# Kernel optimization log

Hardware: AMD Instinct MI355X
Metric: run time of the kernel (lower is better)

Reference implementation:

```python
import jax, jax.numpy as jnp
import numpy as np

B, L, D, K = 32, 128, 400, 40
RTOL, ATOL = 1e-4, 1e-6


def setup_inputs() -> dict:
    key = jax.random.key(0)
    ks = jax.random.split(key, 9)
    s = 0.3                      # input scale keeps exp(energy) in fp32 range
    u = 1.0 / np.sqrt(D)         # param scale
    input_h = jax.random.normal(ks[0], (B, L, D), jnp.float32) * s
    input_c = jax.random.normal(ks[1], (B, L, D), jnp.float32) * s
    W_d = jax.random.normal(ks[2], (K, D), jnp.float32) * u
    W_e = jax.random.normal(ks[3], (K, D), jnp.float32) * u
    U = jax.random.normal(ks[4], (K, D, D), jnp.float32) * u
    b = jax.random.normal(ks[5], (K,), jnp.float32) * 0.1
    heads = jax.random.randint(ks[6], (B, L), 0, L)
    pos = jnp.arange(L)[None, :]
    heads = jnp.where(heads == pos, (heads + 1) % L, heads)  # no self-loops (diag is -inf)
    arc_tags = jax.random.randint(ks[7], (B, L), 0, K)
    lengths = jax.random.randint(ks[8], (B,), L // 2, L + 1)
    mask = (jnp.arange(L)[None, :] < lengths[:, None]).astype(jnp.float32)
    return {"input_h": input_h, "input_c": input_c, "W_d": W_d, "W_e": W_e,
            "U": U, "b": b, "mask": mask, "heads": heads,
            "arc_tags": arc_tags, "lengths": lengths}


def reference(input_h, input_c, W_d, W_e, U, b, mask, heads, arc_tags, lengths):
    Bsz, Ln, _ = input_h.shape
    # --- BiAAttention: energy[b,k,head,child] ---
    bil = jnp.einsum('bhd,kde,bce->bkhc', input_h, U, input_c)
    sd = jnp.einsum('kd,bhd->bkh', W_d, input_h)[:, :, :, None]   # head bias
    se = jnp.einsum('kd,bcd->bkc', W_e, input_c)[:, :, None, :]   # child bias
    energy = bil + sd + se + b[None, :, None, None]
    energy = energy * mask[:, None, :, None] * mask[:, None, None, :]
    eye = jnp.eye(Ln, dtype=energy.dtype)
    energy = energy + jnp.where(eye > 0, -jnp.inf, 0.0)           # no self-arcs
    # --- Matrix-Tree partition function ---
    A = jnp.exp(energy) * mask[:, None, :, None] * mask[:, None, None, :]
    A = A.sum(axis=1)                                             # [B,L,L] over labels
    Dg = A.sum(axis=1) * (1.0 + RTOL) + ATOL                      # column (in-degree) sums
    Lap = eye * Dg[:, None, :] - A                                # Laplacian
    Sub = Lap[:, 1:, 1:]                                          # drop root row/col
    valid = jnp.arange(Ln - 1)[None, :] < (lengths - 1)[:, None]
    vm = valid[:, :, None] & valid[:, None, :]
    Sub = jnp.where(vm, Sub, jnp.eye(Ln - 1, dtype=Sub.dtype))    # identity-pad = logdet of [1:len,1:len]
    z = jnp.linalg.slogdet(Sub)[1]                                # [B]
    # --- gold-tree energy ---
    bi = jnp.arange(Bsz)[:, None]
    pos = jnp.arange(Ln)[None, :]
    te = energy[bi, arc_tags, heads, pos]                         # [B,L]
    tgt = te[:, 1:].sum(axis=1)
    return z - tgt
```

## Files before the change

### kernel.cpp

```cpp
#include <hip/hip_runtime.h>
#include <hip/hip_bf16.h>

#define BB 32
#define LL 128
#define DD 400
#define KK 40
#define EE 416
#define SDN 50
#define SEN 52

typedef __attribute__((ext_vector_type(8)))  short  bfrag;
typedef __attribute__((ext_vector_type(16))) float  ffrag;

static __device__ __forceinline__ short f2bf(float f) {
    union { float f; unsigned u; } v; v.f = f;
    unsigned r = (v.u + 0x7FFF + ((v.u >> 16) & 1)) >> 16;
    return (short)r;
}

__global__ __launch_bounds__(256) void p_hc(
    const float* __restrict__ H, const float* __restrict__ C,
    short* __restrict__ Hs, short* __restrict__ Cs)
{
    int id = blockIdx.x * 256 + threadIdx.x;
    if (id < BB*SDN*LL) {
        int b = id / (SDN*LL); int r = id % (SDN*LL);
        int sd = r / LL; int h = r % LL;
        const float* src = H + ((size_t)(b*LL + h))*DD + sd*8;
        bfrag v;
#pragma unroll
        for (int j = 0; j < 8; ++j) v[j] = f2bf(src[j]);
        *(bfrag*)(Hs + (size_t)id*8) = v;
    } else {
        id -= BB*SDN*LL;
        int b = id / (SEN*LL); int r = id % (SEN*LL);
        int se = r / LL; int c = r % LL;
        bfrag v;
#pragma unroll
        for (int j = 0; j < 8; ++j) {
            int e = se*8 + j;
            v[j] = (e < DD) ? f2bf(C[((size_t)(b*LL + c))*DD + e]) : (short)0;
        }
        *(bfrag*)(Cs + (size_t)id*8) = v;
    }
}

__global__ __launch_bounds__(256) void p_u(
    const float* __restrict__ U, short* __restrict__ Us)
{
    int id = blockIdx.x * 256 + threadIdx.x;
    int k = id / (SDN*EE); int r = id % (SDN*EE);
    int sd = r / EE; int e = r % EE;
    bfrag v;
#pragma unroll
    for (int j = 0; j < 8; ++j)
        v[j] = (e < DD) ? f2bf(U[((size_t)k*DD + sd*8 + j)*DD + e]) : (short)0;
    *(bfrag*)(Us + (size_t)id*8) = v;
}

__global__ __launch_bounds__(256) void k_sdse(
    const float* __restrict__ H, const float* __restrict__ C,
    const float* __restrict__ Wd, const float* __restrict__ We,
    float* __restrict__ SD, float* __restrict__ SE)
{
    const int k = blockIdx.x % KK;
    const int b = blockIdx.x / KK;
    const int t = threadIdx.x;
    __shared__ float wd[DD], we[DD];
    for (int f = t; f < DD; f += 256) { wd[f] = Wd[k*DD + f]; we[f] = We[k*DD + f]; }
    __syncthreads();
    const int row = t & 127;
    const float* src = (t < 128) ? (H + (size_t)(b*LL + row)*DD)
                                 : (C + (size_t)(b*LL + row)*DD);
    const float* w = (t < 128) ? wd : we;
    float s = 0.f;
    for (int d = 0; d < DD; d += 4) {
        float4 v = *(const float4*)(src + d);
        s = fmaf(v.x, w[d+0], s); s = fmaf(v.y, w[d+1], s);
        s = fmaf(v.z, w[d+2], s); s = fmaf(v.w, w[d+3], s);
    }
    if (t < 128) SD[(b*KK + k)*LL + row] = s;
    else         SE[(b*KK + k)*LL + row] = s;
}

__global__ __launch_bounds__(256, 2) void k_mfma(
    const short* __restrict__ Hs, const short* __restrict__ Cs,
    const short* __restrict__ Us,
    const float* __restrict__ SD, const float* __restrict__ SE,
    const float* __restrict__ bvec, const float* __restrict__ mask,
    const int* __restrict__ heads, const int* __restrict__ tags,
    float* __restrict__ A8, float* __restrict__ tgt)
{
    const int k = blockIdx.x;
    const int b = blockIdx.y;
    const int t = threadIdx.x;
    const int w  = t >> 6;
    const int l  = t & 63;
    const int l31 = l & 31;
    const int kh  = l >> 5;
    const int wm  = w >> 1;
    const int wn  = w & 1;

    __shared__ short Tbuf[16*LL*8];

    ffrag Sacc[2][2];
#pragma unroll
    for (int a = 0; a < 2; ++a)
#pragma unroll
        for (int c2 = 0; c2 < 2; ++c2)
#pragma unroll
            for (int r = 0; r < 16; ++r) Sacc[a][c2][r] = 0.f;

    const size_t usK = (size_t)k * SDN * EE;
    const size_t hsB = (size_t)b * SDN * LL;
    const size_t csB = (size_t)b * SEN * LL;

    for (int chunk = 0; chunk < 4; ++chunk) {
        const int e0  = chunk * 128;
        const int NEc = (chunk < 3) ? 128 : 32;
        const int nmt = (NEc == 128) ? 2 : ((wm == 0) ? 1 : 0);

        ffrag Tacc[2][2];
#pragma unroll
        for (int a = 0; a < 2; ++a)
#pragma unroll
            for (int c2 = 0; c2 < 2; ++c2)
#pragma unroll
                for (int r = 0; r < 16; ++r) Tacc[a][c2][r] = 0.f;

        if (nmt > 0) {
            for (int ds = 0; ds < 25; ++ds) {
                const int sdl = 2*ds + kh;
                bfrag afr[2], bfr[2];
#pragma unroll
                for (int mt = 0; mt < 2; ++mt) {
                    if (mt < nmt) {
                        int eg = e0 + 64*wm + 32*mt + l31;
                        afr[mt] = *(const bfrag*)(Us + (usK + (size_t)sdl*EE + eg)*8);
                    }
                }
#pragma unroll
                for (int nt = 0; nt < 2; ++nt) {
                    int h = 64*wn + 32*nt + l31;
                    bfr[nt] = *(const bfrag*)(Hs + (hsB + (size_t)sdl*LL + h)*8);
                }
#pragma unroll
                for (int mt = 0; mt < 2; ++mt) {
                    if (mt < nmt) {
#pragma unroll
                        for (int nt = 0; nt < 2; ++nt)
                            Tacc[mt][nt] = __builtin_amdgcn_mfma_f32_32x32x16_bf16(
                                afr[mt], bfr[nt], Tacc[mt][nt], 0, 0, 0);
                    }
                }
            }
#pragma unroll
            for (int mt = 0; mt < 2; ++mt) {
                if (mt < nmt) {
#pragma unroll
                    for (int nt = 0; nt < 2; ++nt) {
                        int h = 64*wn + 32*nt + l31;
#pragma unroll
                        for (int r = 0; r < 16; r += 2) {
                            int e_loc = 64*wm + 32*mt + (r&3) + 8*(r>>2) + 4*kh;
                            int s_e = e_loc >> 3, e7 = e_loc & 7;
                            unsigned lo = (unsigned short)f2bf(Tacc[mt][nt][r]);
                            unsigned hi = (unsigned short)f2bf(Tacc[mt][nt][r+1]);
                            *(unsigned*)(&Tbuf[((size_t)s_e*LL + h)*8 + e7]) =
                                lo | (hi << 16);
                        }
                    }
                }
            }
        }
        __syncthreads();

        const int esteps = NEc >> 4;
        for (int es = 0; es < esteps; ++es) {
            const int sel = 2*es + kh;
            bfrag afr[2], bfr[2];
#pragma unroll
            for (int at = 0; at < 2; ++at) {
                int h = 64*wm + 32*at + l31;
                afr[at] = *(const bfrag*)(&Tbuf[((size_t)sel*LL + h)*8]);
            }
#pragma unroll
            for (int bt = 0; bt < 2; ++bt) {
                int c = 64*wn + 32*bt + l31;
                int seg = (e0 >> 3) + sel;
                bfr[bt] = *(const bfrag*)(Cs + (csB + (size_t)seg*LL + c)*8);
            }
#pragma unroll
            for (int at = 0; at < 2; ++at)
#pragma unroll
                for (int bt = 0; bt < 2; ++bt)
                    Sacc[at][bt] = __builtin_amdgcn_mfma_f32_32x32x16_bf16(
                        afr[at], bfr[bt], Sacc[at][bt], 0, 0, 0);
        }
        __syncthreads();
    }

    const float bk = bvec[k];
    const float* SDb = SD + ((size_t)b*KK + k)*LL;
    const float* SEb = SE + ((size_t)b*KK + k)*LL;
    float* Ab = A8 + ((size_t)((k & 7)*BB + b))*LL*LL;

#pragma unroll
    for (int at = 0; at < 2; ++at) {
#pragma unroll
        for (int bt = 0; bt < 2; ++bt) {
            const int c = 64*wn + 32*bt + l31;
            const float mc = mask[b*LL + c];
            const float sev = SEb[c];
            const int headc = heads[b*LL + c];
            const int tagc  = tags[b*LL + c];
#pragma unroll
            for (int r = 0; r < 16; ++r) {
                int h = 64*wm + 32*at + (r&3) + 8*(r>>2) + 4*kh;
                if (h == c) continue;
                float mh = mask[b*LL + h];
                if (mh == 0.f || mc == 0.f) continue;
                float eng = Sacc[at][bt][r] + SDb[h] + sev + bk;
                atomicAdd(&Ab[h*LL + c], __expf(eng));
                if (c >= 1 && tagc == k && headc == h) atomicAdd(&tgt[b], eng);
            }
        }
    }
}

__global__ __launch_bounds__(256) void k_logdet(
    const float* __restrict__ A8, const int* __restrict__ lengths,
    const float* __restrict__ tgt, float* __restrict__ out)
{
    const int b = blockIdx.x;
    const int t = threadIdx.x;
    const int rg = t >> 4;
    const int cg = t & 15;

    __shared__ float As[LL*LL];
    __shared__ float Dg[128];
    __shared__ float Lbuf[128];
    __shared__ float Ubuf[128];
    __shared__ float red[256];

    const float4* A4 = (const float4*)A8;
    for (int f4 = t; f4 < 4096; f4 += 256) {
        float4 s = make_float4(0.f, 0.f, 0.f, 0.f);
#pragma unroll
        for (int g = 0; g < 8; ++g) {
            float4 v = A4[((size_t)(g*BB + b))*4096 + f4];
            s.x += v.x; s.y += v.y; s.z += v.z; s.w += v.w;
        }
        ((float4*)As)[f4] = s;
    }
    __syncthreads();

    if (t < 128) {
        float s = 0.f;
        for (int hr = 0; hr < LL; ++hr) s += As[hr*LL + t];
        Dg[t] = s * (1.0f + 1e-4f) + 1e-6f;
    }
    __syncthreads();

    const int n1 = lengths[b] - 1;
    float m[8][8];
#pragma unroll
    for (int r = 0; r < 8; ++r) {
        const int i = 8*rg + r;
#pragma unroll
        for (int c = 0; c < 8; ++c) {
            const int j = 8*cg + c;
            float v;
            if (i < n1 && j < n1)
                v = ((i == j) ? Dg[i+1] : 0.f) - As[(i+1)*LL + (j+1)];
            else
                v = (i == j) ? 1.f : 0.f;
            m[r][c] = v;
        }
    }
    __syncthreads();

    for (int j = 0; j < 127; ++j) {
        const int jg = j >> 3, jl = j & 7;
        if (cg == jg) {
#pragma unroll
            for (int c = 0; c < 8; ++c) {
                if (c == jl) {
#pragma unroll
                    for (int r = 0; r < 8; ++r) Lbuf[8*rg + r] = m[r][c];
                }
            }
        }
        if (rg == jg) {
#pragma unroll
            for (int r = 0; r < 8; ++r) {
                if (r == jl) {
#pragma unroll
                    for (int c = 0; c < 8; ++c) Ubuf[8*cg + c] = m[r][c];
                }
            }
        }
        __syncthreads();

        const float piv = Lbuf[j];
        if (t == j) Dg[j] = piv;
        const float rp = 1.0f / piv;
        float lr[8], ur[8];
#pragma unroll
        for (int r = 0; r < 8; ++r) lr[r] = Lbuf[8*rg + r] * rp;
#pragma unroll
        for (int c = 0; c < 8; ++c) ur[c] = Ubuf[8*cg + c];
#pragma unroll
        for (int r = 0; r < 8; ++r)
#pragma unroll
            for (int c = 0; c < 8; ++c)
                m[r][c] = fmaf(-lr[r], ur[c], m[r][c]);
        __syncthreads();
    }

    float lsum = 0.f;
    if (t < 127) lsum = logf(Dg[t]);
    red[t] = lsum;
    __syncthreads();
    for (int off = 128; off >= 1; off >>= 1) {
        if (t < off) red[t] += red[t + off];
        __syncthreads();
    }
    if (t == 0) out[b] = red[0] - tgt[b];
}

extern "C" void kernel_launch(void* const* d_in, const int* in_sizes, int n_in,
                              void* d_out, int out_size, void* d_ws, size_t ws_size,
                              hipStream_t stream) {
    const float* H    = (const float*)d_in[0];
    const float* C    = (const float*)d_in[1];
    const float* Wd   = (const float*)d_in[2];
    const float* We   = (const float*)d_in[3];
    const float* U    = (const float*)d_in[4];
    const float* bv   = (const float*)d_in[5];
    const float* mask = (const float*)d_in[6];
    const int* heads  = (const int*)d_in[7];
    const int* tags   = (const int*)d_in[8];
    const int* lens   = (const int*)d_in[9];
    float* out = (float*)d_out;

    char* p = (char*)d_ws;
    float* A8  = (float*)p;                 p += (size_t)8*BB*LL*LL*4;
    float* tgt = (float*)p;                 p += 32*4;
    float* SDp = (float*)p;                 p += (size_t)BB*KK*LL*4;
    float* SEp = (float*)p;                 p += (size_t)BB*KK*LL*4;
    short* Hsp = (short*)p;                 p += (size_t)BB*SDN*LL*8*2;
    short* Csp = (short*)p;                 p += (size_t)BB*SEN*LL*8*2;
    short* Usp = (short*)p;                 p += (size_t)KK*SDN*EE*8*2;

    hipMemsetAsync(d_ws, 0, ((size_t)8*BB*LL*LL + 32)*4, stream);

    p_hc  <<<dim3(1632), 256, 0, stream>>>(H, C, Hsp, Csp);
    p_u   <<<dim3(3250), 256, 0, stream>>>(U, Usp);
    k_sdse<<<dim3(BB*KK), 256, 0, stream>>>(H, C, Wd, We, SDp, SEp);
    k_mfma<<<dim3(KK, BB), 256, 0, stream>>>(Hsp, Csp, Usp, SDp, SEp, bv, mask,
                                             heads, tags, A8, tgt);
    k_logdet<<<dim3(BB), 256, 0, stream>>>(A8, lens, tgt, out);
}
```

Before: 413.7 us.

## Merge prep kernels, remap mfma block order, split A-sum into parallel kernel

Merges the three preprocessing kernels (H/C bf16 conversion, U conversion, SD/SE bias dot products) into one launch that branches on block index, removing two launch gaps. The mfma grid is flattened and blocks are remapped so consecutive blocks spread over label groups, which changes how the atomic adds into the 8 A partial copies contend and how work lands on CUs. The 8-way partial-sum reduction that k_logdet did with only 32 blocks moves into a separate 512-block kernel. k_logdet then reads the pre-summed matrix, at the cost of an extra buffer and an extra launch.

Result: slower. 457.4 us (+10.6%).

```diff
diff --git a/kernel.cpp b/kernel.cpp
--- a/kernel.cpp
+++ b/kernel.cpp
@@ -18,69 +18,68 @@
     return (short)r;
 }
 
-__global__ __launch_bounds__(256) void p_hc(
+__global__ __launch_bounds__(256) void k_prep(
     const float* __restrict__ H, const float* __restrict__ C,
-    short* __restrict__ Hs, short* __restrict__ Cs)
-{
-    int id = blockIdx.x * 256 + threadIdx.x;
-    if (id < BB*SDN*LL) {
-        int b = id / (SDN*LL); int r = id % (SDN*LL);
-        int sd = r / LL; int h = r % LL;
-        const float* src = H + ((size_t)(b*LL + h))*DD + sd*8;
-        bfrag v;
-#pragma unroll
-        for (int j = 0; j < 8; ++j) v[j] = f2bf(src[j]);
-        *(bfrag*)(Hs + (size_t)id*8) = v;
-    } else {
-        id -= BB*SDN*LL;
-        int b = id / (SEN*LL); int r = id % (SEN*LL);
-        int se = r / LL; int c = r % LL;
-        bfrag v;
-#pragma unroll
-        for (int j = 0; j < 8; ++j) {
-            int e = se*8 + j;
-            v[j] = (e < DD) ? f2bf(C[((size_t)(b*LL + c))*DD + e]) : (short)0;
-        }
-        *(bfrag*)(Cs + (size_t)id*8) = v;
-    }
-}
-
-__global__ __launch_bounds__(256) void p_u(
-    const float* __restrict__ U, short* __restrict__ Us)
-{
-    int id = blockIdx.x * 256 + threadIdx.x;
-    int k = id / (SDN*EE); int r = id % (SDN*EE);
-    int sd = r / EE; int e = r % EE;
-    bfrag v;
-#pragma unroll
-    for (int j = 0; j < 8; ++j)
-        v[j] = (e < DD) ? f2bf(U[((size_t)k*DD + sd*8 + j)*DD + e]) : (short)0;
-    *(bfrag*)(Us + (size_t)id*8) = v;
-}
-
-__global__ __launch_bounds__(256) void k_sdse(
-    const float* __restrict__ H, const float* __restrict__ C,
+    const float* __restrict__ U,
     const float* __restrict__ Wd, const float* __restrict__ We,
+    short* __restrict__ Hs, short* __restrict__ Cs, short* __restrict__ Us,
     float* __restrict__ SD, float* __restrict__ SE)
 {
-    const int k = blockIdx.x % KK;
-    const int b = blockIdx.x / KK;
+    const int bid = blockIdx.x;
     const int t = threadIdx.x;
-    __shared__ float wd[DD], we[DD];
-    for (int f = t; f < DD; f += 256) { wd[f] = Wd[k*DD + f]; we[f] = We[k*DD + f]; }
-    __syncthreads();
-    const int row = t & 127;
-    const float* src = (t < 128) ? (H + (size_t)(b*LL + row)*DD)
-                                 : (C + (size_t)(b*LL + row)*DD);
-    const float* w = (t < 128) ? wd : we;
-    float s = 0.f;
-    for (int d = 0; d < DD; d += 4) {
-        float4 v = *(const float4*)(src + d);
-        s = fmaf(v.x, w[d+0], s); s = fmaf(v.y, w[d+1], s);
-        s = fmaf(v.z, w[d+2], s); s = fmaf(v.w, w[d+3], s);
-    }
-    if (t < 128) SD[(b*KK + k)*LL + row] = s;
-    else         SE[(b*KK + k)*LL + row] = s;
+    __shared__ float wsh[2*DD];
+
+    if (bid < 1632) {
+        int id = bid * 256 + t;
+        if (id < BB*SDN*LL) {
+            int b = id / (SDN*LL); int r = id % (SDN*LL);
+            int sd = r / LL; int h = r % LL;
+            const float* src = H + ((size_t)(b*LL + h))*DD + sd*8;
+            bfrag v;
+#pragma unroll
+            for (int j = 0; j < 8; ++j) v[j] = f2bf(src[j]);
+            *(bfrag*)(Hs + (size_t)id*8) = v;
+        } else {
+            id -= BB*SDN*LL;
+            int b = id / (SEN*LL); int r = id % (SEN*LL);
+            int se = r / LL; int c = r % LL;
+            bfrag v;
+#pragma unroll
+            for (int j = 0; j < 8; ++j) {
+                int e = se*8 + j;
+                v[j] = (e < DD) ? f2bf(C[((size_t)(b*LL + c))*DD + e]) : (short)0;
+            }
+            *(bfrag*)(Cs + (size_t)id*8) = v;
+        }
+    } else if (bid < 4882) {
+        int id = (bid - 1632) * 256 + t;
+        int k = id / (SDN*EE); int r = id % (SDN*EE);
+        int sd = r / EE; int e = r % EE;
+        bfrag v;
+#pragma unroll
+        for (int j = 0; j < 8; ++j)
+            v[j] = (e < DD) ? f2bf(U[((size_t)k*DD + sd*8 + j)*DD + e]) : (short)0;
+        *(bfrag*)(Us + (size_t)id*8) = v;
+    } else {
+        int sb = bid - 4882;
+        const int k = sb % KK;
+        const int b = sb / KK;
+        float* wd = wsh; float* we = wsh + DD;
+        for (int f = t; f < DD; f += 256) { wd[f] = Wd[k*DD + f]; we[f] = We[k*DD + f]; }
+        __syncthreads();
+        const int row = t & 127;
+        const float* src = (t < 128) ? (H + (size_t)(b*LL + row)*DD)
+                                     : (C + (size_t)(b*LL + row)*DD);
+        const float* w = (t < 128) ? wd : we;
+        float s = 0.f;
+        for (int d = 0; d < DD; d += 4) {
+            float4 v = *(const float4*)(src + d);
+            s = fmaf(v.x, w[d+0], s); s = fmaf(v.y, w[d+1], s);
+            s = fmaf(v.z, w[d+2], s); s = fmaf(v.w, w[d+3], s);
+        }
+        if (t < 128) SD[(b*KK + k)*LL + row] = s;
+        else         SE[(b*KK + k)*LL + row] = s;
+    }
 }
 
 __global__ __launch_bounds__(256, 2) void k_mfma(
@@ -91,8 +90,10 @@
     const int* __restrict__ heads, const int* __restrict__ tags,
     float* __restrict__ A8, float* __restrict__ tgt)
 {
-    const int k = blockIdx.x;
-    const int b = blockIdx.y;
+    const int id = blockIdx.x;
+    const int slot = id >> 3;
+    const int k = (id & 7) * 5 + (slot >> 5);
+    const int b = slot & 31;
     const int t = threadIdx.x;
     const int w  = t >> 6;
     const int l  = t & 63;
@@ -228,8 +229,22 @@
     }
 }
 
+__global__ __launch_bounds__(256) void k_asum(
+    const float4* __restrict__ A8, float4* __restrict__ As)
+{
+    const int f4 = blockIdx.x * 256 + threadIdx.x;
+    const int b = f4 >> 12, r = f4 & 4095;
+    float4 s = make_float4(0.f, 0.f, 0.f, 0.f);
+#pragma unroll
+    for (int g = 0; g < 8; ++g) {
+        float4 v = A8[((size_t)(g*BB + b))*4096 + r];
+        s.x += v.x; s.y += v.y; s.z += v.z; s.w += v.w;
+    }
+    As[f4] = s;
+}
+
 __global__ __launch_bounds__(256) void k_logdet(
-    const float* __restrict__ A8, const int* __restrict__ lengths,
+    const float* __restrict__ Asg, const int* __restrict__ lengths,
     const float* __restrict__ tgt, float* __restrict__ out)
 {
     const int b = blockIdx.x;
@@ -243,16 +258,9 @@
     __shared__ float Ubuf[128];
     __shared__ float red[256];
 
-    const float4* A4 = (const float4*)A8;
-    for (int f4 = t; f4 < 4096; f4 += 256) {
-        float4 s = make_float4(0.f, 0.f, 0.f, 0.f);
-#pragma unroll
-        for (int g = 0; g < 8; ++g) {
-            float4 v = A4[((size_t)(g*BB + b))*4096 + f4];
-            s.x += v.x; s.y += v.y; s.z += v.z; s.w += v.w;
-        }
-        ((float4*)As)[f4] = s;
-    }
+    const float4* As4 = (const float4*)Asg;
+    for (int f4 = t; f4 < 4096; f4 += 256)
+        ((float4*)As)[f4] = As4[(size_t)b*4096 + f4];
     __syncthreads();
 
     if (t < 128) {
@@ -347,6 +355,7 @@
     char* p = (char*)d_ws;
     float* A8  = (float*)p;                 p += (size_t)8*BB*LL*LL*4;
     float* tgt = (float*)p;                 p += 32*4;
+    float* As  = (float*)p;                 p += (size_t)BB*LL*LL*4;
     float* SDp = (float*)p;                 p += (size_t)BB*KK*LL*4;
     float* SEp = (float*)p;                 p += (size_t)BB*KK*LL*4;
     short* Hsp = (short*)p;                 p += (size_t)BB*SDN*LL*8*2;
@@ -355,10 +364,9 @@
 
     hipMemsetAsync(d_ws, 0, ((size_t)8*BB*LL*LL + 32)*4, stream);
 
-    p_hc  <<<dim3(1632), 256, 0, stream>>>(H, C, Hsp, Csp);
-    p_u   <<<dim3(3250), 256, 0, stream>>>(U, Usp);
-    k_sdse<<<dim3(BB*KK), 256, 0, stream>>>(H, C, Wd, We, SDp, SEp);
-    k_mfma<<<dim3(KK, BB), 256, 0, stream>>>(Hsp, Csp, Usp, SDp, SEp, bv, mask,
-                                             heads, tags, A8, tgt);
-    k_logdet<<<dim3(BB), 256, 0, stream>>>(A8, lens, tgt, out);
-}
+    k_prep<<<dim3(6162), 256, 0, stream>>>(H, C, U, Wd, We, Hsp, Csp, Usp, SDp, SEp);
+    k_mfma<<<dim3(KK*BB), 256, 0, stream>>>(Hsp, Csp, Usp, SDp, SEp, bv, mask,
+                                            heads, tags, A8, tgt);
+    k_asum<<<dim3(512), 256, 0, stream>>>((const float4*)A8, (float4*)As);
+    k_logdet<<<dim3(BB), 256, 0, stream>>>(As, lens, tgt, out);
+}
```

## Split fused bilinear MFMA kernel into separate T and S GEMM kernels

Applied to the files above, without the earlier changes.

Replaces the single per-(k,b) kernel, which computed U·H into shared memory chunk by chunk and then multiplied by C, with two kernels: k_T writes the bf16 intermediate T to global memory and k_S multiplies it by C. Both use 16x16x32 MFMA tiles with register double-buffered loads, and they run over K in two halves to bound the workspace. Padding is extended to 512/52 so the loops have no edge branches. The 8-way A reduction also moves out of k_logdet into a grid-wide kernel. In exchange it adds global-memory traffic for T, more launches, and some padded MFMA work.

New measurement: 444.4 us. +7.4%, slower.

```diff
diff --git a/kernel.cpp b/kernel.cpp
--- a/kernel.cpp
+++ b/kernel.cpp
@@ -5,34 +5,41 @@
 #define LL 128
 #define DD 400
 #define KK 40
-#define EE 416
-#define SDN 50
+#define SDN 52
 #define SEN 52
-
-typedef __attribute__((ext_vector_type(8)))  short  bfrag;
-typedef __attribute__((ext_vector_type(16))) float  ffrag;
+#define EP 512
+#define KHALF 20
+
+typedef __attribute__((ext_vector_type(8))) short bfrag;
+typedef __attribute__((ext_vector_type(4))) float cfrag;
 
 static __device__ __forceinline__ short f2bf(float f) {
     union { float f; unsigned u; } v; v.f = f;
     unsigned r = (v.u + 0x7FFF + ((v.u >> 16) & 1)) >> 16;
     return (short)r;
 }
+static __device__ __forceinline__ unsigned pack2(float a, float b) {
+    return (unsigned)(unsigned short)f2bf(a) | ((unsigned)(unsigned short)f2bf(b) << 16);
+}
 
 __global__ __launch_bounds__(256) void p_hc(
     const float* __restrict__ H, const float* __restrict__ C,
     short* __restrict__ Hs, short* __restrict__ Cs)
 {
     int id = blockIdx.x * 256 + threadIdx.x;
-    if (id < BB*SDN*LL) {
+    const int NH = BB*SDN*LL;
+    if (id < NH) {
         int b = id / (SDN*LL); int r = id % (SDN*LL);
         int sd = r / LL; int h = r % LL;
-        const float* src = H + ((size_t)(b*LL + h))*DD + sd*8;
         bfrag v;
 #pragma unroll
-        for (int j = 0; j < 8; ++j) v[j] = f2bf(src[j]);
+        for (int j = 0; j < 8; ++j) {
+            int d = sd*8 + j;
+            v[j] = (d < DD) ? f2bf(H[((size_t)(b*LL + h))*DD + d]) : (short)0;
+        }
         *(bfrag*)(Hs + (size_t)id*8) = v;
-    } else {
-        id -= BB*SDN*LL;
+    } else if (id < 2*NH) {
+        id -= NH;
         int b = id / (SEN*LL); int r = id % (SEN*LL);
         int se = r / LL; int c = r % LL;
         bfrag v;
@@ -49,12 +56,15 @@
     const float* __restrict__ U, short* __restrict__ Us)
 {
     int id = blockIdx.x * 256 + threadIdx.x;
-    int k = id / (SDN*EE); int r = id % (SDN*EE);
-    int sd = r / EE; int e = r % EE;
+    if (id >= KK*SDN*EP) return;
+    int k = id / (SDN*EP); int r = id % (SDN*EP);
+    int sd = r / EP; int e = r % EP;
     bfrag v;
 #pragma unroll
-    for (int j = 0; j < 8; ++j)
-        v[j] = (e < DD) ? f2bf(U[((size_t)k*DD + sd*8 + j)*DD + e]) : (short)0;
+    for (int j = 0; j < 8; ++j) {
+        int d = sd*8 + j;
+        v[j] = (d < DD && e < DD) ? f2bf(U[((size_t)k*DD + d)*DD + e]) : (short)0;
+    }
     *(bfrag*)(Us + (size_t)id*8) = v;
 }
 
@@ -83,153 +93,183 @@
     else         SE[(b*KK + k)*LL + row] = s;
 }
 
-__global__ __launch_bounds__(256, 2) void k_mfma(
-    const short* __restrict__ Hs, const short* __restrict__ Cs,
-    const short* __restrict__ Us,
+__global__ __launch_bounds__(256, 2) void k_T(
+    const short* __restrict__ Us, const short* __restrict__ Hs,
+    short* __restrict__ Tb, int k0)
+{
+    const int et = blockIdx.x;
+    const int b  = blockIdx.y;
+    const int kz = blockIdx.z;
+    const int kk = k0 + kz;
+    const int t = threadIdx.x;
+    const int w = t >> 6, l = t & 63;
+    const int wr = w >> 1, wc = w & 1;
+    const int l15 = l & 15, l4 = l >> 4;
+
+    const int m0 = et*128 + wr*64;
+    const int n0 = wc*64;
+
+    const bfrag* A = (const bfrag*)(Us + (size_t)kk*SDN*EP*8);
+    const bfrag* Bv = (const bfrag*)(Hs + (size_t)b*SDN*LL*8);
+
+    cfrag acc[4][4];
+#pragma unroll
+    for (int i = 0; i < 4; ++i)
+#pragma unroll
+        for (int j = 0; j < 4; ++j)
+#pragma unroll
+            for (int r = 0; r < 4; ++r) acc[i][j][r] = 0.f;
+
+    bfrag af[4], bf[4];
+#pragma unroll
+    for (int i = 0; i < 4; ++i) {
+        af[i] = A[l4*EP + m0 + i*16 + l15];
+        bf[i] = Bv[l4*LL + n0 + i*16 + l15];
+    }
+    for (int sdc = 0; sdc < 13; ++sdc) {
+        bfrag afn[4], bfn[4];
+        if (sdc < 12) {
+            const int sdn = (sdc + 1)*4 + l4;
+#pragma unroll
+            for (int i = 0; i < 4; ++i) {
+                afn[i] = A[sdn*EP + m0 + i*16 + l15];
+                bfn[i] = Bv[sdn*LL + n0 + i*16 + l15];
+            }
+        } else {
+#pragma unroll
+            for (int i = 0; i < 4; ++i) { afn[i] = af[i]; bfn[i] = bf[i]; }
+        }
+#pragma unroll
+        for (int mf = 0; mf < 4; ++mf)
+#pragma unroll
+            for (int nf = 0; nf < 4; ++nf)
+                acc[mf][nf] = __builtin_amdgcn_mfma_f32_16x16x32_bf16(
+                    af[mf], bf[nf], acc[mf][nf], 0, 0, 0);
+#pragma unroll
+        for (int i = 0; i < 4; ++i) { af[i] = afn[i]; bf[i] = bfn[i]; }
+    }
+
+    short* To = Tb + (size_t)(kz*BB + b)*SEN*LL*8;
+#pragma unroll
+    for (int mf = 0; mf < 4; ++mf) {
+        const int e0 = m0 + mf*16 + l4*4;
+        if (e0 < 416) {
+            const int se = e0 >> 3, e7 = e0 & 7;
+#pragma unroll
+            for (int nf = 0; nf < 4; ++nf) {
+                const int h = n0 + nf*16 + l15;
+                uint2 pv;
+                pv.x = pack2(acc[mf][nf][0], acc[mf][nf][1]);
+                pv.y = pack2(acc[mf][nf][2], acc[mf][nf][3]);
+                *(uint2*)(To + (size_t)(se*LL + h)*8 + e7) = pv;
+            }
+        }
+    }
+}
+
+__global__ __launch_bounds__(256, 2) void k_S(
+    const short* __restrict__ Tb, const short* __restrict__ Cs,
     const float* __restrict__ SD, const float* __restrict__ SE,
     const float* __restrict__ bvec, const float* __restrict__ mask,
     const int* __restrict__ heads, const int* __restrict__ tags,
-    float* __restrict__ A8, float* __restrict__ tgt)
-{
-    const int k = blockIdx.x;
-    const int b = blockIdx.y;
+    float* __restrict__ A8, float* __restrict__ tgt, int k0)
+{
+    const int kz = blockIdx.x;
+    const int kk = k0 + kz;
+    const int b  = blockIdx.y;
     const int t = threadIdx.x;
-    const int w  = t >> 6;
-    const int l  = t & 63;
-    const int l31 = l & 31;
-    const int kh  = l >> 5;
-    const int wm  = w >> 1;
-    const int wn  = w & 1;
-
-    __shared__ short Tbuf[16*LL*8];
-
-    ffrag Sacc[2][2];
-#pragma unroll
-    for (int a = 0; a < 2; ++a)
-#pragma unroll
-        for (int c2 = 0; c2 < 2; ++c2)
-#pragma unroll
-            for (int r = 0; r < 16; ++r) Sacc[a][c2][r] = 0.f;
-
-    const size_t usK = (size_t)k * SDN * EE;
-    const size_t hsB = (size_t)b * SDN * LL;
-    const size_t csB = (size_t)b * SEN * LL;
-
-    for (int chunk = 0; chunk < 4; ++chunk) {
-        const int e0  = chunk * 128;
-        const int NEc = (chunk < 3) ? 128 : 32;
-        const int nmt = (NEc == 128) ? 2 : ((wm == 0) ? 1 : 0);
-
-        ffrag Tacc[2][2];
-#pragma unroll
-        for (int a = 0; a < 2; ++a)
-#pragma unroll
-            for (int c2 = 0; c2 < 2; ++c2)
-#pragma unroll
-                for (int r = 0; r < 16; ++r) Tacc[a][c2][r] = 0.f;
-
-        if (nmt > 0) {
-            for (int ds = 0; ds < 25; ++ds) {
-                const int sdl = 2*ds + kh;
-                bfrag afr[2], bfr[2];
-#pragma unroll
-                for (int mt = 0; mt < 2; ++mt) {
-                    if (mt < nmt) {
-                        int eg = e0 + 64*wm + 32*mt + l31;
-                        afr[mt] = *(const bfrag*)(Us + (usK + (size_t)sdl*EE + eg)*8);
-                    }
-                }
-#pragma unroll
-                for (int nt = 0; nt < 2; ++nt) {
-                    int h = 64*wn + 32*nt + l31;
-                    bfr[nt] = *(const bfrag*)(Hs + (hsB + (size_t)sdl*LL + h)*8);
-                }
-#pragma unroll
-                for (int mt = 0; mt < 2; ++mt) {
-                    if (mt < nmt) {
-#pragma unroll
-                        for (int nt = 0; nt < 2; ++nt)
-                            Tacc[mt][nt] = __builtin_amdgcn_mfma_f32_32x32x16_bf16(
-                                afr[mt], bfr[nt], Tacc[mt][nt], 0, 0, 0);
-                    }
-                }
-            }
-#pragma unroll
-            for (int mt = 0; mt < 2; ++mt) {
-                if (mt < nmt) {
-#pragma unroll
-                    for (int nt = 0; nt < 2; ++nt) {
-                        int h = 64*wn + 32*nt + l31;
-#pragma unroll
-                        for (int r = 0; r < 16; r += 2) {
-                            int e_loc = 64*wm + 32*mt + (r&3) + 8*(r>>2) + 4*kh;
-                            int s_e = e_loc >> 3, e7 = e_loc & 7;
-                            unsigned lo = (unsigned short)f2bf(Tacc[mt][nt][r]);
-                            unsigned hi = (unsigned short)f2bf(Tacc[mt][nt][r+1]);
-                            *(unsigned*)(&Tbuf[((size_t)s_e*LL + h)*8 + e7]) =
-                                lo | (hi << 16);
-                        }
-                    }
-                }
-            }
-        }
-        __syncthreads();
-
-        const int esteps = NEc >> 4;
-        for (int es = 0; es < esteps; ++es) {
-            const int sel = 2*es + kh;
-            bfrag afr[2], bfr[2];
-#pragma unroll
-            for (int at = 0; at < 2; ++at) {
-                int h = 64*wm + 32*at + l31;
-                afr[at] = *(const bfrag*)(&Tbuf[((size_t)sel*LL + h)*8]);
-            }
-#pragma unroll
-            for (int bt = 0; bt < 2; ++bt) {
-                int c = 64*wn + 32*bt + l31;
-                int seg = (e0 >> 3) + sel;
-                bfr[bt] = *(const bfrag*)(Cs + (csB + (size_t)seg*LL + c)*8);
-            }
-#pragma unroll
-            for (int at = 0; at < 2; ++at)
-#pragma unroll
-                for (int bt = 0; bt < 2; ++bt)
-                    Sacc[at][bt] = __builtin_amdgcn_mfma_f32_32x32x16_bf16(
-                        afr[at], bfr[bt], Sacc[at][bt], 0, 0, 0);
-        }
-        __syncthreads();
-    }
-
-    const float bk = bvec[k];
-    const float* SDb = SD + ((size_t)b*KK + k)*LL;
-    const float* SEb = SE + ((size_t)b*KK + k)*LL;
-    float* Ab = A8 + ((size_t)((k & 7)*BB + b))*LL*LL;
-
-#pragma unroll
-    for (int at = 0; at < 2; ++at) {
-#pragma unroll
-        for (int bt = 0; bt < 2; ++bt) {
-            const int c = 64*wn + 32*bt + l31;
-            const float mc = mask[b*LL + c];
-            const float sev = SEb[c];
-            const int headc = heads[b*LL + c];
-            const int tagc  = tags[b*LL + c];
-#pragma unroll
-            for (int r = 0; r < 16; ++r) {
-                int h = 64*wm + 32*at + (r&3) + 8*(r>>2) + 4*kh;
+    const int w = t >> 6, l = t & 63;
+    const int wr = w >> 1, wc = w & 1;
+    const int l15 = l & 15, l4 = l >> 4;
+
+    const int h0 = wr*64;
+    const int c0 = wc*64;
+
+    const bfrag* A = (const bfrag*)(Tb + (size_t)(kz*BB + b)*SEN*LL*8);
+    const bfrag* Bv = (const bfrag*)(Cs + (size_t)b*SEN*LL*8);
+
+    cfrag acc[4][4];
+#pragma unroll
+    for (int i = 0; i < 4; ++i)
+#pragma unroll
+        for (int j = 0; j < 4; ++j)
+#pragma unroll
+            for (int r = 0; r < 4; ++r) acc[i][j][r] = 0.f;
+
+    bfrag af[4], bf[4];
+#pragma unroll
+    for (int i = 0; i < 4; ++i) {
+        af[i] = A[l4*LL + h0 + i*16 + l15];
+        bf[i] = Bv[l4*LL + c0 + i*16 + l15];
+    }
+    for (int esc = 0; esc < 13; ++esc) {
+        bfrag afn[4], bfn[4];
+        if (esc < 12) {
+            const int sen = (esc + 1)*4 + l4;
+#pragma unroll
+            for (int i = 0; i < 4; ++i) {
+                afn[i] = A[sen*LL + h0 + i*16 + l15];
+                bfn[i] = Bv[sen*LL + c0 + i*16 + l15];
+            }
+        } else {
+#pragma unroll
+            for (int i = 0; i < 4; ++i) { afn[i] = af[i]; bfn[i] = bf[i]; }
+        }
+#pragma unroll
+        for (int mf = 0; mf < 4; ++mf)
+#pragma unroll
+            for (int nf = 0; nf < 4; ++nf)
+                acc[mf][nf] = __builtin_amdgcn_mfma_f32_16x16x32_bf16(
+                    af[mf], bf[nf], acc[mf][nf], 0, 0, 0);
+#pragma unroll
+        for (int i = 0; i < 4; ++i) { af[i] = afn[i]; bf[i] = bfn[i]; }
+    }
+
+    const float bk = bvec[kk];
+    const float* SDb = SD + ((size_t)b*KK + kk)*LL;
+    const float* SEb = SE + ((size_t)b*KK + kk)*LL;
+    float* Ab = A8 + (size_t)((kk & 7)*BB + b)*LL*LL;
+
+#pragma unroll
+    for (int nf = 0; nf < 4; ++nf) {
+        const int c = c0 + nf*16 + l15;
+        const float mc = mask[b*LL + c];
+        const float sev = SEb[c];
+        const int headc = heads[b*LL + c];
+        const int tagc  = tags[b*LL + c];
+#pragma unroll
+        for (int mf = 0; mf < 4; ++mf) {
+            const int hb = h0 + mf*16 + l4*4;
+#pragma unroll
+            for (int r = 0; r < 4; ++r) {
+                const int h = hb + r;
                 if (h == c) continue;
-                float mh = mask[b*LL + h];
+                const float mh = mask[b*LL + h];
                 if (mh == 0.f || mc == 0.f) continue;
-                float eng = Sacc[at][bt][r] + SDb[h] + sev + bk;
+                float eng = acc[mf][nf][r] + SDb[h] + sev + bk;
                 atomicAdd(&Ab[h*LL + c], __expf(eng));
-                if (c >= 1 && tagc == k && headc == h) atomicAdd(&tgt[b], eng);
-            }
-        }
-    }
+                if (c >= 1 && tagc == kk && headc == h) atomicAdd(&tgt[b], eng);
+            }
+        }
+    }
+}
+
+__global__ __launch_bounds__(256) void k_asum(
+    const float4* __restrict__ A8, float4* __restrict__ As)
+{
+    const int f4 = blockIdx.x * 256 + threadIdx.x;
+    const int b = f4 >> 12, r = f4 & 4095;
+    float4 s = make_float4(0.f, 0.f, 0.f, 0.f);
+#pragma unroll
+    for (int g = 0; g < 8; ++g) {
+        float4 v = A8[((size_t)(g*BB + b))*4096 + r];
+        s.x += v.x; s.y += v.y; s.z += v.z; s.w += v.w;
+    }
+    As[f4] = s;
 }
 
 __global__ __launch_bounds__(256) void k_logdet(
-    const float* __restrict__ A8, const int* __restrict__ lengths,
+    const float* __restrict__ Asg, const int* __restrict__ lengths,
     const float* __restrict__ tgt, float* __restrict__ out)
 {
     const int b = blockIdx.x;
@@ -243,16 +283,9 @@
     __shared__ float Ubuf[128];
     __shared__ float red[256];
 
-    const float4* A4 = (const float4*)A8;
-    for (int f4 = t; f4 < 4096; f4 += 256) {
-        float4 s = make_float4(0.f, 0.f, 0.f, 0.f);
-#pragma unroll
-        for (int g = 0; g < 8; ++g) {
-            float4 v = A4[((size_t)(g*BB + b))*4096 + f4];
-            s.x += v.x; s.y += v.y; s.z += v.z; s.w += v.w;
-        }
-        ((float4*)As)[f4] = s;
-    }
+    const float4* As4 = (const float4*)Asg;
+    for (int f4 = t; f4 < 4096; f4 += 256)
+        ((float4*)As)[f4] = As4[(size_t)b*4096 + f4];
     __syncthreads();
 
     if (t < 128) {
@@ -346,19 +379,28 @@
 
     char* p = (char*)d_ws;
     float* A8  = (float*)p;                 p += (size_t)8*BB*LL*LL*4;
-    float* tgt = (float*)p;                 p += 32*4;
+    float* tgt = (float*)p;                 p += 128*4;
+    float* As  = (float*)p;                 p += (size_t)BB*LL*LL*4;
     float* SDp = (float*)p;                 p += (size_t)BB*KK*LL*4;
     float* SEp = (float*)p;                 p += (size_t)BB*KK*LL*4;
     short* Hsp = (short*)p;                 p += (size_t)BB*SDN*LL*8*2;
     short* Csp = (short*)p;                 p += (size_t)BB*SEN*LL*8*2;
-    short* Usp = (short*)p;                 p += (size_t)KK*SDN*EE*8*2;
-
-    hipMemsetAsync(d_ws, 0, ((size_t)8*BB*LL*LL + 32)*4, stream);
-
-    p_hc  <<<dim3(1632), 256, 0, stream>>>(H, C, Hsp, Csp);
-    p_u   <<<dim3(3250), 256, 0, stream>>>(U, Usp);
+    short* Usp = (short*)p;                 p += (size_t)KK*SDN*EP*8*2;
+    short* Tbp = (short*)p;                 p += (size_t)KHALF*BB*SEN*LL*8*2;
+
+    hipMemsetAsync(d_ws, 0, ((size_t)8*BB*LL*LL + 128)*4, stream);
+
+    p_hc  <<<dim3(1664), 256, 0, stream>>>(H, C, Hsp, Csp);
+    p_u   <<<dim3(4160), 256, 0, stream>>>(U, Usp);
     k_sdse<<<dim3(BB*KK), 256, 0, stream>>>(H, C, Wd, We, SDp, SEp);
-    k_mfma<<<dim3(KK, BB), 256, 0, stream>>>(Hsp, Csp, Usp, SDp, SEp, bv, mask,
-                                             heads, tags, A8, tgt);
-    k_logdet<<<dim3(BB), 256, 0, stream>>>(A8, lens, tgt, out);
-}
+
+    for (int half = 0; half < 2; ++half) {
+        const int k0 = half * KHALF;
+        k_T<<<dim3(4, BB, KHALF), 256, 0, stream>>>(Usp, Hsp, Tbp, k0);
+        k_S<<<dim3(KHALF, BB), 256, 0, stream>>>(Tbp, Csp, SDp, SEp, bv, mask,
+                                                 heads, tags, A8, tgt, k0);
+    }
+
+    k_asum<<<dim3(512), 256, 0, stream>>>((const float4*)A8, (float4*)As);
+    k_logdet<<<dim3(BB), 256, 0, stream>>>(As, lens, tgt, out);
+}
```
